# Performance work log

Hardware: AMD Instinct MI355X
Metric: run time of the kernel (lower is better)

Reference implementation:

```python
import jax, jax.numpy as jnp
import numpy as np

B, T, C = 2, 2048, 1024
H = 16
D = C // H  # head_dim = 64
SCALE = D ** -0.5


def setup_inputs() -> dict:
    key = jax.random.key(0)
    ks = jax.random.split(key, 5)
    s = 0.02
    return {
        "x": jax.random.normal(ks[0], (B, T, C), dtype=jnp.float32),
        "w_qkv": jax.random.normal(ks[1], (C, 3 * C), dtype=jnp.float32) * s,
        "b_qkv": jnp.zeros((3 * C,), dtype=jnp.float32),
        "w_proj": jax.random.normal(ks[2], (C, C), dtype=jnp.float32) * s,
        "b_proj": jnp.zeros((C,), dtype=jnp.float32),
    }


def reference(x, w_qkv, b_qkv, w_proj, b_proj):
    Bx, Tx, Cx = x.shape
    qkv = x @ w_qkv + b_qkv                      # [B,T,3C]
    q, k, v = jnp.split(qkv, 3, axis=-1)
    # [B,T,C] -> [B,H,T,D]
    q = q.reshape(Bx, Tx, H, D).transpose(0, 2, 1, 3)
    k = k.reshape(Bx, Tx, H, D).transpose(0, 2, 1, 3)
    v = v.reshape(Bx, Tx, H, D).transpose(0, 2, 1, 3)
    attn = jnp.einsum('bhqd,bhkd->bhqk', q, k) * SCALE
    causal = jnp.tril(jnp.ones((Tx, Tx), dtype=bool))
    attn = jnp.where(causal[None, None], attn, -jnp.inf)
    attn = jax.nn.softmax(attn, axis=-1)
    out = jnp.einsum('bhqk,bhkd->bhqd', attn, v)  # [B,H,T,D]
    out = out.transpose(0, 2, 1, 3).reshape(Bx, Tx, Cx)
    return out @ w_proj + b_proj
```

## Files before the change

### kernel.cpp

```cpp
#include <hip/hip_runtime.h>
#include <hip/hip_bf16.h>
#include <math.h>

#define T_SEQ 2048
#define NHEAD 16
#define HDIM  64
#define CDIM  1024
#define KDIM  1024
#define SCALE_L2E 0.1803368801111204f

typedef __attribute__((ext_vector_type(8))) short bf16x8;
typedef __attribute__((ext_vector_type(4))) float f32x4;
typedef __attribute__((ext_vector_type(16))) float f32x16;
typedef __attribute__((ext_vector_type(8))) unsigned short u16x8;
typedef __attribute__((ext_vector_type(4))) unsigned int u32x4;

__device__ __forceinline__ unsigned short f2bf(float f) {
    unsigned int u = __builtin_bit_cast(unsigned int, f);
    u += 0x7fffu + ((u >> 16) & 1u);
    return (unsigned short)(u >> 16);
}
__device__ __forceinline__ unsigned int cvt_pk_bf16(float lo, float hi_) {
    unsigned int r;
    asm("v_cvt_pk_bf16_f32 %0, %1, %2" : "=v"(r) : "v"(lo), "v"(hi_));
    return r;
}
__device__ __forceinline__ void pl32swap(unsigned int &a, unsigned int &b) {
    asm("v_permlane32_swap_b32 %0, %1" : "+v"(a), "+v"(b));
}
__device__ __forceinline__ void gld16(const unsigned short* g, unsigned short* l) {
    __builtin_amdgcn_global_load_lds(
        (const __attribute__((address_space(1))) unsigned int*)g,
        (__attribute__((address_space(3))) unsigned int*)l,
        16, 0, 0);
}

__global__ __launch_bounds__(256) void prep_x(const float* __restrict__ x,
                                              unsigned short* __restrict__ Xb) {
    size_t i = ((size_t)blockIdx.x * 256 + threadIdx.x) * 8;
    float4 a = *(const float4*)(x + i);
    float4 b = *(const float4*)(x + i + 4);
    u32x4 o;
    o[0] = cvt_pk_bf16(a.x, a.y);
    o[1] = cvt_pk_bf16(a.z, a.w);
    o[2] = cvt_pk_bf16(b.x, b.y);
    o[3] = cvt_pk_bf16(b.z, b.w);
    *(u32x4*)(Xb + i) = o;
}

template<int NC>
__global__ __launch_bounds__(256) void prep_w(const float* __restrict__ W,
                                              unsigned short* __restrict__ Wt) {
    __shared__ unsigned short Ls[64][72];
    const int n0 = blockIdx.x * 64, k0 = blockIdx.y * 64;
    const int t = threadIdx.x;
    {
        int kr = t >> 2, nc = (t & 3) * 16;
        #pragma unroll
        for (int j = 0; j < 4; j++) {
            float4 v = *(const float4*)(W + (size_t)(k0 + kr) * NC + n0 + nc + j * 4);
            Ls[nc + j*4 + 0][kr] = f2bf(v.x);
            Ls[nc + j*4 + 1][kr] = f2bf(v.y);
            Ls[nc + j*4 + 2][kr] = f2bf(v.z);
            Ls[nc + j*4 + 3][kr] = f2bf(v.w);
        }
    }
    __syncthreads();
    {
        int nr = t >> 2, kc = (t & 3) * 16;
        u16x8 o0 = *(const u16x8*)&Ls[nr][kc];
        u16x8 o1 = *(const u16x8*)&Ls[nr][kc + 8];
        *(u16x8*)(Wt + (size_t)(n0 + nr) * KDIM + k0 + kc)     = o0;
        *(u16x8*)(Wt + (size_t)(n0 + nr) * KDIM + k0 + kc + 8) = o1;
    }
}

template<int NC, int EPI>
__global__ __launch_bounds__(256) void gemm_k(
    const unsigned short* __restrict__ A, const unsigned short* __restrict__ Wt,
    const float* __restrict__ bias, float* __restrict__ Of,
    unsigned short* __restrict__ Qb, unsigned short* __restrict__ Kb,
    unsigned short* __restrict__ Vt)
{
    __shared__ unsigned short As[128 * 64];
    __shared__ unsigned short Bs[128 * 64];

    const int tid  = threadIdx.x;
    const int lane = tid & 63;
    const int wid  = tid >> 6;
    const int m0 = blockIdx.x * 128;
    const int n0 = blockIdx.y * 128;
    const int wm = (wid >> 1) * 64;
    const int wn = (wid & 1) * 64;
    const int rl = lane & 15;

    const int r8 = lane >> 3, s8 = lane & 7;
    const int swzs = (s8 ^ r8) * 8;

    f32x4 acc[4][4] = {};

    for (int k0 = 0; k0 < KDIM; k0 += 64) {
        #pragma unroll
        for (int c = 0; c < 4; c++) {
            int row = (wid << 5) + (c << 3) + r8;
            gld16(A  + (size_t)(m0 + row) * KDIM + k0 + swzs, &As[(size_t)((wid<<5)+(c<<3)) * 64]);
            gld16(Wt + (size_t)(n0 + row) * KDIM + k0 + swzs, &Bs[(size_t)((wid<<5)+(c<<3)) * 64]);
        }
        __syncthreads();
        #pragma unroll
        for (int kc = 0; kc < 2; kc++) {
            const int sb = kc * 4 + (lane >> 4);
            bf16x8 af[4], bfr[4];
            #pragma unroll
            for (int f = 0; f < 4; f++) {
                int sw = (sb ^ (rl & 7)) * 8;
                af[f]  = *(const bf16x8*)&As[(wm + f*16 + rl) * 64 + sw];
                bfr[f] = *(const bf16x8*)&Bs[(wn + f*16 + rl) * 64 + sw];
            }
            __builtin_amdgcn_s_setprio(1);
            #pragma unroll
            for (int i = 0; i < 4; i++)
                #pragma unroll
                for (int j = 0; j < 4; j++)
                    acc[i][j] = __builtin_amdgcn_mfma_f32_16x16x32_bf16(af[i], bfr[j], acc[i][j], 0, 0, 0);
            __builtin_amdgcn_s_setprio(0);
        }
        __syncthreads();
    }

    #pragma unroll
    for (int j = 0; j < 4; j++) {
        int gn = n0 + wn + j*16 + rl;
        float bv = bias[gn];
        #pragma unroll
        for (int i = 0; i < 4; i++) {
            int gm0 = m0 + wm + i*16 + (lane >> 4) * 4;
            #pragma unroll
            for (int r = 0; r < 4; r++) {
                float v = acc[i][j][r] + bv;
                int gm = gm0 + r;
                if (EPI == 0) {
                    int which = gn >> 10;
                    int cw = gn & 1023;
                    int h = cw >> 6, d = cw & 63;
                    int b = gm >> 11, t = gm & 2047;
                    size_t bh = (size_t)(b * NHEAD + h);
                    if (which == 0)      Qb[(bh * T_SEQ + t) * HDIM + d] = f2bf(v * SCALE_L2E);
                    else if (which == 1) Kb[(bh * T_SEQ + t) * HDIM + d] = f2bf(v);
                    else                 Vt[(bh * HDIM + d) * T_SEQ + t] = f2bf(v);
                } else {
                    Of[(size_t)gm * NC + gn] = v;
                }
            }
        }
    }
}

__global__ __launch_bounds__(256) void attn_k(
    const unsigned short* __restrict__ Qb, const unsigned short* __restrict__ Kb,
    const unsigned short* __restrict__ Vt, unsigned short* __restrict__ AO)
{
    __shared__ unsigned short sbuf[3 * 8192];

    const int tid  = threadIdx.x;
    const int lane = tid & 63;
    const int w    = tid >> 6;
    const int bh   = blockIdx.x;
    const int qt   = 15 - blockIdx.y;
    const int q0w  = qt * 128 + w * 32;
    const int ql   = lane & 31;
    const int hi   = lane >> 5;
    const int qg   = q0w + ql;
    const int nt   = 2 * qt + 2;

    const unsigned short* Qp = Qb + (size_t)bh * T_SEQ * HDIM;
    const unsigned short* Kp = Kb + (size_t)bh * T_SEQ * HDIM;
    const unsigned short* Vp = Vt + (size_t)bh * HDIM * T_SEQ;

    const int r8 = lane >> 3, s8 = lane & 7;
    const int swzs = (s8 ^ r8) * 8;
    const unsigned short* sp0;
    size_t stepE, cstep;
    int dstbase;
    if (w < 2) {
        sp0 = Kp + (size_t)((w << 5) + r8) * HDIM + swzs;
        stepE = 64 * HDIM; cstep = 8 * HDIM;
        dstbase = (w << 5) * 64;
    } else {
        sp0 = Vp + (size_t)(((w - 2) << 5) + r8) * T_SEQ + swzs;
        stepE = 64; cstep = 8 * T_SEQ;
        dstbase = 4096 + (((w - 2) << 5)) * 64;
    }

    bf16x8 qf[4];
    #pragma unroll
    for (int dc = 0; dc < 4; dc++)
        qf[dc] = *(const bf16x8*)(Qp + (size_t)qg * HDIM + dc*16 + hi*8);
    asm volatile("s_waitcnt vmcnt(0)" ::: "memory");

    float m_run = -INFINITY, l_run = 0.f;
    f32x16 o0 = {}, o1 = {};

    #pragma unroll
    for (int pt = 0; pt < 3; pt++) {
        int ct = pt < nt ? pt : nt - 1;
        #pragma unroll
        for (int c = 0; c < 4; c++)
            gld16(sp0 + (size_t)ct * stepE + c * cstep,
                  &sbuf[pt * 8192 + dstbase + c * 512]);
    }

    int bsel = 0;
    for (int t = 0; t < nt; ++t) {
        const int c0 = t << 6;
        asm volatile("s_waitcnt vmcnt(8)" ::: "memory");
        __builtin_amdgcn_s_barrier();
        __builtin_amdgcn_sched_barrier(0);

        if (c0 <= q0w) {
            const char* kb = (const char*)&sbuf[bsel * 8192];
            const char* vb = kb + 8192;
            const bool a1 = (c0 + 32 <= q0w);

            f32x16 s0 = {}, s1 = {};
            __builtin_amdgcn_s_setprio(1);
            #pragma unroll
            for (int dc = 0; dc < 4; dc++) {
                int sw = (((dc << 1) | hi) ^ (ql & 7)) << 4;
                bf16x8 kf = *(const bf16x8*)(kb + ql*128 + sw);
                s0 = __builtin_amdgcn_mfma_f32_32x32x16_bf16(kf, qf[dc], s0, 0, 0, 0);
            }
            if (a1) {
                #pragma unroll
                for (int dc = 0; dc < 4; dc++) {
                    int sw = (((dc << 1) | hi) ^ (ql & 7)) << 4;
                    bf16x8 kf = *(const bf16x8*)(kb + 4096 + ql*128 + sw);
                    s1 = __builtin_amdgcn_mfma_f32_32x32x16_bf16(kf, qf[dc], s1, 0, 0, 0);
                }
            }
            __builtin_amdgcn_s_setprio(0);

            float pm0[16], pm1[16];
            #pragma unroll
            for (int r = 0; r < 16; r++) { pm0[r] = s0[r]; pm1[r] = s1[r]; }
            if (c0 == q0w) {
                #pragma unroll
                for (int r = 0; r < 16; r++) {
                    int kv = c0 + (r & 3) + 8 * (r >> 2) + 4 * hi;
                    pm0[r] = (kv > qg) ? -INFINITY : pm0[r];
                }
            }
            if (a1 && (c0 + 32 == q0w)) {
                #pragma unroll
                for (int r = 0; r < 16; r++) {
                    int kv = c0 + 32 + (r & 3) + 8 * (r >> 2) + 4 * hi;
                    pm1[r] = (kv > qg) ? -INFINITY : pm1[r];
                }
            }

            float tm = pm0[0];
            #pragma unroll
            for (int r = 1; r < 16; r++) tm = fmaxf(tm, pm0[r]);
            if (a1) {
                #pragma unroll
                for (int r = 0; r < 16; r++) tm = fmaxf(tm, pm1[r]);
            }
            tm = fmaxf(tm, __shfl_xor(tm, 32));
            if (__any(tm > m_run + 11.5f)) {
                float mn = fmaxf(m_run, tm);
                float sf = exp2f(m_run - mn);
                m_run = mn;
                l_run *= sf;
                #pragma unroll
                for (int r = 0; r < 16; r++) { o0[r] *= sf; o1[r] *= sf; }
            }
            float p0[16], p1[16]; float rs = 0.f;
            #pragma unroll
            for (int r = 0; r < 16; r++) { p0[r] = exp2f(pm0[r] - m_run); rs += p0[r]; }
            if (a1) {
                #pragma unroll
                for (int r = 0; r < 16; r++) { p1[r] = exp2f(pm1[r] - m_run); rs += p1[r]; }
            }
            rs += __shfl_xor(rs, 32);
            l_run += rs;

            const int swv0 = ((0 + hi) ^ (ql & 7)) << 4;
            const int swv1 = ((2 + hi) ^ (ql & 7)) << 4;
            const int swv2 = ((4 + hi) ^ (ql & 7)) << 4;
            const int swv3 = ((6 + hi) ^ (ql & 7)) << 4;
            const char* vrow0 = vb + ql * 128;
            const char* vrow1 = vb + (32 + ql) * 128;

            unsigned int c[8];
            #pragma unroll
            for (int i = 0; i < 8; i++) c[i] = cvt_pk_bf16(p0[2*i], p0[2*i+1]);
            pl32swap(c[0], c[2]);  pl32swap(c[1], c[3]);
            pl32swap(c[4], c[6]);  pl32swap(c[5], c[7]);
            u32x4 b0 = {c[0], c[1], c[2], c[3]};
            u32x4 b1 = {c[4], c[5], c[6], c[7]};
            bf16x8 pf0 = __builtin_bit_cast(bf16x8, b0);
            bf16x8 pf1 = __builtin_bit_cast(bf16x8, b1);

            bf16x8 v00 = *(const bf16x8*)(vrow0 + swv0);
            bf16x8 v01 = *(const bf16x8*)(vrow0 + swv1);
            bf16x8 v10 = *(const bf16x8*)(vrow1 + swv0);
            bf16x8 v11 = *(const bf16x8*)(vrow1 + swv1);
            __builtin_amdgcn_s_setprio(1);
            o0 = __builtin_amdgcn_mfma_f32_32x32x16_bf16(v00, pf0, o0, 0, 0, 0);
            o0 = __builtin_amdgcn_mfma_f32_32x32x16_bf16(v01, pf1, o0, 0, 0, 0);
            o1 = __builtin_amdgcn_mfma_f32_32x32x16_bf16(v10, pf0, o1, 0, 0, 0);
            o1 = __builtin_amdgcn_mfma_f32_32x32x16_bf16(v11, pf1, o1, 0, 0, 0);
            __builtin_amdgcn_s_setprio(0);

            if (a1) {
                #pragma unroll
                for (int i = 0; i < 8; i++) c[i] = cvt_pk_bf16(p1[2*i], p1[2*i+1]);
                pl32swap(c[0], c[2]);  pl32swap(c[1], c[3]);
                pl32swap(c[4], c[6]);  pl32swap(c[5], c[7]);
                u32x4 b2 = {c[0], c[1], c[2], c[3]};
                u32x4 b3 = {c[4], c[5], c[6], c[7]};
                bf16x8 pf2 = __builtin_bit_cast(bf16x8, b2);
                bf16x8 pf3 = __builtin_bit_cast(bf16x8, b3);
                bf16x8 v02 = *(const bf16x8*)(vrow0 + swv2);
                bf16x8 v03 = *(const bf16x8*)(vrow0 + swv3);
                bf16x8 v12 = *(const bf16x8*)(vrow1 + swv2);
                bf16x8 v13 = *(const bf16x8*)(vrow1 + swv3);
                __builtin_amdgcn_s_setprio(1);
                o0 = __builtin_amdgcn_mfma_f32_32x32x16_bf16(v02, pf2, o0, 0, 0, 0);
                o0 = __builtin_amdgcn_mfma_f32_32x32x16_bf16(v03, pf3, o0, 0, 0, 0);
                o1 = __builtin_amdgcn_mfma_f32_32x32x16_bf16(v12, pf2, o1, 0, 0, 0);
                o1 = __builtin_amdgcn_mfma_f32_32x32x16_bf16(v13, pf3, o1, 0, 0, 0);
                __builtin_amdgcn_s_setprio(0);
            }
        }

        __builtin_amdgcn_sched_barrier(0);
        __builtin_amdgcn_s_barrier();
        int ct = t + 3; if (ct > nt - 1) ct = nt - 1;
        #pragma unroll
        for (int cch = 0; cch < 4; cch++)
            gld16(sp0 + (size_t)ct * stepE + cch * cstep,
                  &sbuf[bsel * 8192 + dstbase + cch * 512]);
        if (++bsel == 3) bsel = 0;
    }

    const float inv_l = 1.f / l_run;
    const int b = bh >> 4, h = bh & 15;
    unsigned short* aop = AO + ((size_t)(b * T_SEQ + qg)) * CDIM + h * HDIM;
    #pragma unroll
    for (int qd = 0; qd < 4; qd++) {
        uint2 w0, w1;
        w0.x = cvt_pk_bf16(o0[4*qd+0] * inv_l, o0[4*qd+1] * inv_l);
        w0.y = cvt_pk_bf16(o0[4*qd+2] * inv_l, o0[4*qd+3] * inv_l);
        w1.x = cvt_pk_bf16(o1[4*qd+0] * inv_l, o1[4*qd+1] * inv_l);
        w1.y = cvt_pk_bf16(o1[4*qd+2] * inv_l, o1[4*qd+3] * inv_l);
        *(uint2*)(aop + qd*8 + hi*4)      = w0;
        *(uint2*)(aop + 32 + qd*8 + hi*4) = w1;
    }
}

extern "C" void kernel_launch(void* const* d_in, const int* in_sizes, int n_in,
                              void* d_out, int out_size, void* d_ws, size_t ws_size,
                              hipStream_t stream) {
    const float* x      = (const float*)d_in[0];
    const float* w_qkv  = (const float*)d_in[1];
    const float* b_qkv  = (const float*)d_in[2];
    const float* w_proj = (const float*)d_in[3];
    const float* b_proj = (const float*)d_in[4];
    float* out = (float*)d_out;

    const size_t MI = (size_t)1 << 20;
    unsigned short* base = (unsigned short*)d_ws;
    unsigned short* Qb  = base;
    unsigned short* Kb  = base + 4*MI;
    unsigned short* Vt  = base + 8*MI;
    unsigned short* Wqt = base + 12*MI;
    unsigned short* Wpt = base + 15*MI;
    unsigned short* Xb  = base + 16*MI;
    unsigned short* AO  = Xb;

    prep_x<<<dim3(2048), 256, 0, stream>>>(x, Xb);
    prep_w<3072><<<dim3(48, 16), 256, 0, stream>>>(w_qkv, Wqt);
    prep_w<1024><<<dim3(16, 16), 256, 0, stream>>>(w_proj, Wpt);
    gemm_k<3072, 0><<<dim3(32, 24), 256, 0, stream>>>(
        Xb, Wqt, b_qkv, nullptr, Qb, Kb, Vt);
    attn_k<<<dim3(32, 16), 256, 0, stream>>>(Qb, Kb, Vt, AO);
    gemm_k<1024, 1><<<dim3(32, 8), 256, 0, stream>>>(
        AO, Wpt, b_proj, out, nullptr, nullptr, nullptr);
}
```

Baseline: 127.2 us.

## Shrink attention blocks to 64 queries with two warps and double-buffered KV

The attention kernel now uses 128-thread blocks of two warps, each covering 64 query rows, so the grid doubles to 32x32 blocks. The KV pipeline moves from a 3-stage ring with a vmcnt(8) wait to a double buffer where the next tile is issued right after a full vmcnt(0) wait. The per-warp skip of fully masked tiles is dropped because both warps always need every tile up to the diagonal. The goal is smaller per-block LDS, more resident blocks and finer causal load balance. The cost is more redundant K/V loading across blocks and a shallower prefetch, which may expose memory latency.

New measurement: 131.0 us. 1.03x slower.

```diff
diff --git a/kernel.cpp b/kernel.cpp
--- a/kernel.cpp
+++ b/kernel.cpp
@@ -156,22 +156,22 @@
     }
 }
 
-__global__ __launch_bounds__(256) void attn_k(
+__global__ __launch_bounds__(128) void attn_k(
     const unsigned short* __restrict__ Qb, const unsigned short* __restrict__ Kb,
     const unsigned short* __restrict__ Vt, unsigned short* __restrict__ AO)
 {
-    __shared__ unsigned short sbuf[3 * 8192];
+    __shared__ unsigned short sbuf[2 * 8192];
 
     const int tid  = threadIdx.x;
     const int lane = tid & 63;
     const int w    = tid >> 6;
     const int bh   = blockIdx.x;
-    const int qt   = 15 - blockIdx.y;
-    const int q0w  = qt * 128 + w * 32;
+    const int qt   = 31 - blockIdx.y;
+    const int q0w  = qt * 64 + w * 32;
     const int ql   = lane & 31;
     const int hi   = lane >> 5;
     const int qg   = q0w + ql;
-    const int nt   = 2 * qt + 2;
+    const int nt   = qt + 1;
 
     const unsigned short* Qp = Qb + (size_t)bh * T_SEQ * HDIM;
     const unsigned short* Kp = Kb + (size_t)bh * T_SEQ * HDIM;
@@ -182,166 +182,158 @@
     const unsigned short* sp0;
     size_t stepE, cstep;
     int dstbase;
-    if (w < 2) {
-        sp0 = Kp + (size_t)((w << 5) + r8) * HDIM + swzs;
+    if (w == 0) {
+        sp0 = Kp + (size_t)r8 * HDIM + swzs;
         stepE = 64 * HDIM; cstep = 8 * HDIM;
-        dstbase = (w << 5) * 64;
+        dstbase = 0;
     } else {
-        sp0 = Vp + (size_t)(((w - 2) << 5) + r8) * T_SEQ + swzs;
+        sp0 = Vp + (size_t)r8 * T_SEQ + swzs;
         stepE = 64; cstep = 8 * T_SEQ;
-        dstbase = 4096 + (((w - 2) << 5)) * 64;
+        dstbase = 4096;
     }
 
     bf16x8 qf[4];
     #pragma unroll
     for (int dc = 0; dc < 4; dc++)
         qf[dc] = *(const bf16x8*)(Qp + (size_t)qg * HDIM + dc*16 + hi*8);
-    asm volatile("s_waitcnt vmcnt(0)" ::: "memory");
 
     float m_run = -INFINITY, l_run = 0.f;
     f32x16 o0 = {}, o1 = {};
 
     #pragma unroll
-    for (int pt = 0; pt < 3; pt++) {
-        int ct = pt < nt ? pt : nt - 1;
-        #pragma unroll
-        for (int c = 0; c < 4; c++)
-            gld16(sp0 + (size_t)ct * stepE + c * cstep,
-                  &sbuf[pt * 8192 + dstbase + c * 512]);
-    }
-
-    int bsel = 0;
+    for (int c = 0; c < 8; c++)
+        gld16(sp0 + c * cstep, &sbuf[dstbase + c * 512]);
+
     for (int t = 0; t < nt; ++t) {
         const int c0 = t << 6;
-        asm volatile("s_waitcnt vmcnt(8)" ::: "memory");
+        asm volatile("s_waitcnt vmcnt(0)" ::: "memory");
         __builtin_amdgcn_s_barrier();
         __builtin_amdgcn_sched_barrier(0);
 
-        if (c0 <= q0w) {
-            const char* kb = (const char*)&sbuf[bsel * 8192];
-            const char* vb = kb + 8192;
-            const bool a1 = (c0 + 32 <= q0w);
-
-            f32x16 s0 = {}, s1 = {};
-            __builtin_amdgcn_s_setprio(1);
+        if (t + 1 < nt) {
+            #pragma unroll
+            for (int c = 0; c < 8; c++)
+                gld16(sp0 + (size_t)(t + 1) * stepE + c * cstep,
+                      &sbuf[((t + 1) & 1) * 8192 + dstbase + c * 512]);
+        }
+
+        const char* kb = (const char*)sbuf + (t & 1) * 16384;
+        const char* vb = kb + 8192;
+        const bool a1 = (c0 + 32 <= q0w);
+
+        f32x16 s0 = {}, s1 = {};
+        __builtin_amdgcn_s_setprio(1);
+        #pragma unroll
+        for (int dc = 0; dc < 4; dc++) {
+            int sw = (((dc << 1) | hi) ^ (ql & 7)) << 4;
+            bf16x8 kf = *(const bf16x8*)(kb + ql*128 + sw);
+            s0 = __builtin_amdgcn_mfma_f32_32x32x16_bf16(kf, qf[dc], s0, 0, 0, 0);
+        }
+        if (a1) {
             #pragma unroll
             for (int dc = 0; dc < 4; dc++) {
                 int sw = (((dc << 1) | hi) ^ (ql & 7)) << 4;
-                bf16x8 kf = *(const bf16x8*)(kb + ql*128 + sw);
-                s0 = __builtin_amdgcn_mfma_f32_32x32x16_bf16(kf, qf[dc], s0, 0, 0, 0);
-            }
-            if (a1) {
-                #pragma unroll
-                for (int dc = 0; dc < 4; dc++) {
-                    int sw = (((dc << 1) | hi) ^ (ql & 7)) << 4;
-                    bf16x8 kf = *(const bf16x8*)(kb + 4096 + ql*128 + sw);
-                    s1 = __builtin_amdgcn_mfma_f32_32x32x16_bf16(kf, qf[dc], s1, 0, 0, 0);
-                }
-            }
-            __builtin_amdgcn_s_setprio(0);
-
-            float pm0[16], pm1[16];
-            #pragma unroll
-            for (int r = 0; r < 16; r++) { pm0[r] = s0[r]; pm1[r] = s1[r]; }
-            if (c0 == q0w) {
-                #pragma unroll
-                for (int r = 0; r < 16; r++) {
-                    int kv = c0 + (r & 3) + 8 * (r >> 2) + 4 * hi;
-                    pm0[r] = (kv > qg) ? -INFINITY : pm0[r];
-                }
-            }
-            if (a1 && (c0 + 32 == q0w)) {
-                #pragma unroll
-                for (int r = 0; r < 16; r++) {
-                    int kv = c0 + 32 + (r & 3) + 8 * (r >> 2) + 4 * hi;
-                    pm1[r] = (kv > qg) ? -INFINITY : pm1[r];
-                }
-            }
-
-            float tm = pm0[0];
-            #pragma unroll
-            for (int r = 1; r < 16; r++) tm = fmaxf(tm, pm0[r]);
-            if (a1) {
-                #pragma unroll
-                for (int r = 0; r < 16; r++) tm = fmaxf(tm, pm1[r]);
-            }
-            tm = fmaxf(tm, __shfl_xor(tm, 32));
-            if (__any(tm > m_run + 11.5f)) {
-                float mn = fmaxf(m_run, tm);
-                float sf = exp2f(m_run - mn);
-                m_run = mn;
-                l_run *= sf;
-                #pragma unroll
-                for (int r = 0; r < 16; r++) { o0[r] *= sf; o1[r] *= sf; }
-            }
-            float p0[16], p1[16]; float rs = 0.f;
-            #pragma unroll
-            for (int r = 0; r < 16; r++) { p0[r] = exp2f(pm0[r] - m_run); rs += p0[r]; }
-            if (a1) {
-                #pragma unroll
-                for (int r = 0; r < 16; r++) { p1[r] = exp2f(pm1[r] - m_run); rs += p1[r]; }
-            }
-            rs += __shfl_xor(rs, 32);
-            l_run += rs;
-
-            const int swv0 = ((0 + hi) ^ (ql & 7)) << 4;
-            const int swv1 = ((2 + hi) ^ (ql & 7)) << 4;
-            const int swv2 = ((4 + hi) ^ (ql & 7)) << 4;
-            const int swv3 = ((6 + hi) ^ (ql & 7)) << 4;
-            const char* vrow0 = vb + ql * 128;
-            const char* vrow1 = vb + (32 + ql) * 128;
-
-            unsigned int c[8];
-            #pragma unroll
-            for (int i = 0; i < 8; i++) c[i] = cvt_pk_bf16(p0[2*i], p0[2*i+1]);
+                bf16x8 kf = *(const bf16x8*)(kb + 4096 + ql*128 + sw);
+                s1 = __builtin_amdgcn_mfma_f32_32x32x16_bf16(kf, qf[dc], s1, 0, 0, 0);
+            }
+        }
+        __builtin_amdgcn_s_setprio(0);
+
+        float pm0[16], pm1[16];
+        #pragma unroll
+        for (int r = 0; r < 16; r++) { pm0[r] = s0[r]; pm1[r] = s1[r]; }
+        if (c0 == q0w) {
+            #pragma unroll
+            for (int r = 0; r < 16; r++) {
+                int kv = c0 + (r & 3) + 8 * (r >> 2) + 4 * hi;
+                pm0[r] = (kv > qg) ? -INFINITY : pm0[r];
+            }
+        }
+        if (a1 && (c0 + 32 == q0w)) {
+            #pragma unroll
+            for (int r = 0; r < 16; r++) {
+                int kv = c0 + 32 + (r & 3) + 8 * (r >> 2) + 4 * hi;
+                pm1[r] = (kv > qg) ? -INFINITY : pm1[r];
+            }
+        }
+
+        float tm = pm0[0];
+        #pragma unroll
+        for (int r = 1; r < 16; r++) tm = fmaxf(tm, pm0[r]);
+        if (a1) {
+            #pragma unroll
+            for (int r = 0; r < 16; r++) tm = fmaxf(tm, pm1[r]);
+        }
+        tm = fmaxf(tm, __shfl_xor(tm, 32));
+        if (__any(tm > m_run + 11.5f)) {
+            float mn = fmaxf(m_run, tm);
+            float sf = exp2f(m_run - mn);
+            m_run = mn;
+            l_run *= sf;
+            #pragma unroll
+            for (int r = 0; r < 16; r++) { o0[r] *= sf; o1[r] *= sf; }
+        }
+        float p0[16], p1[16]; float rs = 0.f;
+        #pragma unroll
+        for (int r = 0; r < 16; r++) { p0[r] = exp2f(pm0[r] - m_run); rs += p0[r]; }
+        if (a1) {
+            #pragma unroll
+            for (int r = 0; r < 16; r++) { p1[r] = exp2f(pm1[r] - m_run); rs += p1[r]; }
+        }
+        rs += __shfl_xor(rs, 32);
+        l_run += rs;
+
+        const int swv0 = ((0 + hi) ^ (ql & 7)) << 4;
+        const int swv1 = ((2 + hi) ^ (ql & 7)) << 4;
+        const int swv2 = ((4 + hi) ^ (ql & 7)) << 4;
+        const int swv3 = ((6 + hi) ^ (ql & 7)) << 4;
+        const char* vrow0 = vb + ql * 128;
+        const char* vrow1 = vb + (32 + ql) * 128;
+
+        unsigned int c[8];
+        #pragma unroll
+        for (int i = 0; i < 8; i++) c[i] = cvt_pk_bf16(p0[2*i], p0[2*i+1]);
+        pl32swap(c[0], c[2]);  pl32swap(c[1], c[3]);
+        pl32swap(c[4], c[6]);  pl32swap(c[5], c[7]);
+        u32x4 b0 = {c[0], c[1], c[2], c[3]};
+        u32x4 b1 = {c[4], c[5], c[6], c[7]};
+        bf16x8 pf0 = __builtin_bit_cast(bf16x8, b0);
+        bf16x8 pf1 = __builtin_bit_cast(bf16x8, b1);
+
+        bf16x8 v00 = *(const bf16x8*)(vrow0 + swv0);
+        bf16x8 v01 = *(const bf16x8*)(vrow0 + swv1);
+        bf16x8 v10 = *(const bf16x8*)(vrow1 + swv0);
+        bf16x8 v11 = *(const bf16x8*)(vrow1 + swv1);
+        __builtin_amdgcn_s_setprio(1);
+        o0 = __builtin_amdgcn_mfma_f32_32x32x16_bf16(v00, pf0, o0, 0, 0, 0);
+        o0 = __builtin_amdgcn_mfma_f32_32x32x16_bf16(v01, pf1, o0, 0, 0, 0);
+        o1 = __builtin_amdgcn_mfma_f32_32x32x16_bf16(v10, pf0, o1, 0, 0, 0);
+        o1 = __builtin_amdgcn_mfma_f32_32x32x16_bf16(v11, pf1, o1, 0, 0, 0);
+        __builtin_amdgcn_s_setprio(0);
+
+        if (a1) {
+            #pragma unroll
+            for (int i = 0; i < 8; i++) c[i] = cvt_pk_bf16(p1[2*i], p1[2*i+1]);
             pl32swap(c[0], c[2]);  pl32swap(c[1], c[3]);
             pl32swap(c[4], c[6]);  pl32swap(c[5], c[7]);
-            u32x4 b0 = {c[0], c[1], c[2], c[3]};
-            u32x4 b1 = {c[4], c[5], c[6], c[7]};
-            bf16x8 pf0 = __builtin_bit_cast(bf16x8, b0);
-            bf16x8 pf1 = __builtin_bit_cast(bf16x8, b1);
-
-            bf16x8 v00 = *(const bf16x8*)(vrow0 + swv0);
-            bf16x8 v01 = *(const bf16x8*)(vrow0 + swv1);
-            bf16x8 v10 = *(const bf16x8*)(vrow1 + swv0);
-            bf16x8 v11 = *(const bf16x8*)(vrow1 + swv1);
+            u32x4 b2 = {c[0], c[1], c[2], c[3]};
+            u32x4 b3 = {c[4], c[5], c[6], c[7]};
+            bf16x8 pf2 = __builtin_bit_cast(bf16x8, b2);
+            bf16x8 pf3 = __builtin_bit_cast(bf16x8, b3);
+            bf16x8 v02 = *(const bf16x8*)(vrow0 + swv2);
+            bf16x8 v03 = *(const bf16x8*)(vrow0 + swv3);
+            bf16x8 v12 = *(const bf16x8*)(vrow1 + swv2);
+            bf16x8 v13 = *(const bf16x8*)(vrow1 + swv3);
             __builtin_amdgcn_s_setprio(1);
-            o0 = __builtin_amdgcn_mfma_f32_32x32x16_bf16(v00, pf0, o0, 0, 0, 0);
-            o0 = __builtin_amdgcn_mfma_f32_32x32x16_bf16(v01, pf1, o0, 0, 0, 0);
-            o1 = __builtin_amdgcn_mfma_f32_32x32x16_bf16(v10, pf0, o1, 0, 0, 0);
-            o1 = __builtin_amdgcn_mfma_f32_32x32x16_bf16(v11, pf1, o1, 0, 0, 0);
+            o0 = __builtin_amdgcn_mfma_f32_32x32x16_bf16(v02, pf2, o0, 0, 0, 0);
+            o0 = __builtin_amdgcn_mfma_f32_32x32x16_bf16(v03, pf3, o0, 0, 0, 0);
+            o1 = __builtin_amdgcn_mfma_f32_32x32x16_bf16(v12, pf2, o1, 0, 0, 0);
+            o1 = __builtin_amdgcn_mfma_f32_32x32x16_bf16(v13, pf3, o1, 0, 0, 0);
             __builtin_amdgcn_s_setprio(0);
-
-            if (a1) {
-                #pragma unroll
-                for (int i = 0; i < 8; i++) c[i] = cvt_pk_bf16(p1[2*i], p1[2*i+1]);
-                pl32swap(c[0], c[2]);  pl32swap(c[1], c[3]);
-                pl32swap(c[4], c[6]);  pl32swap(c[5], c[7]);
-                u32x4 b2 = {c[0], c[1], c[2], c[3]};
-                u32x4 b3 = {c[4], c[5], c[6], c[7]};
-                bf16x8 pf2 = __builtin_bit_cast(bf16x8, b2);
-                bf16x8 pf3 = __builtin_bit_cast(bf16x8, b3);
-                bf16x8 v02 = *(const bf16x8*)(vrow0 + swv2);
-                bf16x8 v03 = *(const bf16x8*)(vrow0 + swv3);
-                bf16x8 v12 = *(const bf16x8*)(vrow1 + swv2);
-                bf16x8 v13 = *(const bf16x8*)(vrow1 + swv3);
-                __builtin_amdgcn_s_setprio(1);
-                o0 = __builtin_amdgcn_mfma_f32_32x32x16_bf16(v02, pf2, o0, 0, 0, 0);
-                o0 = __builtin_amdgcn_mfma_f32_32x32x16_bf16(v03, pf3, o0, 0, 0, 0);
-                o1 = __builtin_amdgcn_mfma_f32_32x32x16_bf16(v12, pf2, o1, 0, 0, 0);
-                o1 = __builtin_amdgcn_mfma_f32_32x32x16_bf16(v13, pf3, o1, 0, 0, 0);
-                __builtin_amdgcn_s_setprio(0);
-            }
         }
 
         __builtin_amdgcn_sched_barrier(0);
         __builtin_amdgcn_s_barrier();
-        int ct = t + 3; if (ct > nt - 1) ct = nt - 1;
-        #pragma unroll
-        for (int cch = 0; cch < 4; cch++)
-            gld16(sp0 + (size_t)ct * stepE + cch * cstep,
-                  &sbuf[bsel * 8192 + dstbase + cch * 512]);
-        if (++bsel == 3) bsel = 0;
     }
 
     const float inv_l = 1.f / l_run;
@@ -384,7 +376,7 @@
     prep_w<1024><<<dim3(16, 16), 256, 0, stream>>>(w_proj, Wpt);
     gemm_k<3072, 0><<<dim3(32, 24), 256, 0, stream>>>(
         Xb, Wqt, b_qkv, nullptr, Qb, Kb, Vt);
-    attn_k<<<dim3(32, 16), 256, 0, stream>>>(Qb, Kb, Vt, AO);
+    attn_k<<<dim3(32, 32), 128, 0, stream>>>(Qb, Kb, Vt, AO);
     gemm_k<1024, 1><<<dim3(32, 8), 256, 0, stream>>>(
         AO, Wpt, b_proj, out, nullptr, nullptr, nullptr);
 }
```
